# Optimization experiments

Measured on AMD Instinct MI355X. Metric: run time of the kernel, lower is better.

The kernel has to match this reference:

```python
import jax, jax.numpy as jnp
import numpy as np

B, T, IN_DIM, H, W = 32, 20, 3, 1, 256
HID = 64
FC1_IN = HID * T * H * W  # 327680
FC1_OUT = 512
OUT_DIM = 3


def setup_inputs() -> dict:
    key = jax.random.key(0)
    ks = jax.random.split(key, 6)
    s = 0.02
    return dict(
        x=jax.random.normal(ks[0], (B, T, IN_DIM, H, W), dtype=jnp.float32),
        conv_w0=jax.random.normal(ks[1], (4 * HID, IN_DIM + HID, 3, 3), dtype=jnp.float32) * s,
        conv_b0=jnp.zeros((4 * HID,), dtype=jnp.float32),
        conv_w1=jax.random.normal(ks[2], (4 * HID, HID + HID, 3, 3), dtype=jnp.float32) * s,
        conv_b1=jnp.zeros((4 * HID,), dtype=jnp.float32),
        fc1_w=jax.random.normal(ks[3], (FC1_OUT, FC1_IN), dtype=jnp.float32) * s,
        fc1_b=jnp.zeros((FC1_OUT,), dtype=jnp.float32),
        fc2_w=jax.random.normal(ks[4], (OUT_DIM, FC1_OUT), dtype=jnp.float32) * s,
        fc2_b=jnp.zeros((OUT_DIM,), dtype=jnp.float32),
    )


def _convlstm_layer(inp, w, b):
    # inp: (B, T, C, H, W); w: (4*hid, C+hid, kh, kw)
    Bn, Tn, C, Hn, Wn = inp.shape
    hid = w.shape[0] // 4
    h0 = jnp.zeros((Bn, hid, Hn, Wn), inp.dtype)

    def step(carry, x_t):
        h, c = carry
        z = jnp.concatenate([x_t, h], axis=1)  # (B, C+hid, H, W)
        gates = jax.lax.conv_general_dilated(
            z, w, window_strides=(1, 1), padding='SAME',
            dimension_numbers=('NCHW', 'OIHW', 'NCHW')) + b[None, :, None, None]
        i, f, o, g = jnp.split(gates, 4, axis=1)
        c_new = jax.nn.sigmoid(f) * c + jax.nn.sigmoid(i) * jnp.tanh(g)
        h_new = jax.nn.sigmoid(o) * jnp.tanh(c_new)
        return (h_new, c_new), h_new

    _, hs = jax.lax.scan(step, (h0, h0), jnp.swapaxes(inp, 0, 1))
    return jnp.swapaxes(hs, 0, 1)  # (B, T, hid, H, W)


def reference(x, conv_w0, conv_b0, conv_w1, conv_b1, fc1_w, fc1_b, fc2_w, fc2_b):
    h = _convlstm_layer(x, conv_w0, conv_b0)
    h = _convlstm_layer(h, conv_w1, conv_b1)
    flat = h.reshape(h.shape[0], -1)  # (B, T*hid*H*W), torch .view order
    z = jax.nn.relu(flat @ fc1_w.T + fc1_b)
    out = z @ fc2_w.T + fc2_b
    return jnp.concatenate([out[:, :2], jax.nn.sigmoid(out[:, 2:])], axis=1)
```

## Files before the change

kernel.cpp:

```cpp
#include <hip/hip_runtime.h>
#include <hip/hip_bf16.h>
#include <cstddef>

#define BATCH 32
#define TSTEPS 20
#define IN_DIM 3
#define WIDTH 256
#define HID 64
#define FC1_IN 327680
#define FC1_OUT 512
#define OUT_DIM 3

#define MARG 8
#define REGC 48
#define CORE 8
#define ROWS 50
#define CROWS 48

#define KSLICE 1280
#define KPHASE 640
#define NSPLIT 256

typedef _Float16 half8 __attribute__((ext_vector_type(8)));
typedef float floatx4 __attribute__((ext_vector_type(4)));

__device__ __forceinline__ float sigm(float x) {
    return 1.0f / (1.0f + __expf(-x));
}
__device__ __forceinline__ float tanh_fast(float x) {
    return 1.0f - 2.0f / (__expf(2.0f * x) + 1.0f);
}


__global__ __launch_bounds__(256) void prep_w0(
    const float* __restrict__ cw0, _Float16* __restrict__ wt0)
{
    int e = blockIdx.x * 256 + threadIdx.x;
    if (e >= 256 * 96) return;
    int co = e / 96, cip = e - co * 96;
    int ci = (cip < 64) ? (3 + cip) : (cip < 67 ? cip - 64 : -1);
    float v[3] = {0.f, 0.f, 0.f};
    if (ci >= 0) {
#pragma unroll
        for (int kw = 0; kw < 3; ++kw)
            v[kw] = cw0[(size_t)(co * 67 + ci) * 9 + 3 + kw];
    }
#pragma unroll
    for (int kw = 0; kw < 3; ++kw)
        wt0[(size_t)(kw * 256 + co) * 96 + cip] = (_Float16)v[kw];
}

__global__ __launch_bounds__(256) void prep_w1(
    const float* __restrict__ cw1, _Float16* __restrict__ wt1)
{
    int e = blockIdx.x * 256 + threadIdx.x;
    int co = e >> 7, ci = e & 127;
#pragma unroll
    for (int kw = 0; kw < 3; ++kw)
        wt1[(size_t)(kw * 256 + co) * 128 + ci] =
            (_Float16)cw1[(size_t)(co * 128 + ci) * 9 + 3 + kw];
}

__global__ __launch_bounds__(256) void prep_x(
    const float* __restrict__ x, _Float16* __restrict__ xT)
{
    int e = blockIdx.x * 256 + threadIdx.x;
    if (e >= TSTEPS * BATCH * WIDTH) return;
    int t = e / (BATCH * WIDTH);
    int rem = e - t * BATCH * WIDTH;
    int b = rem >> 8, w = rem & 255;
    half8 v = {};
#pragma unroll
    for (int ci = 0; ci < 3; ++ci)
        v[ci] = (_Float16)x[(size_t)((b * TSTEPS + t) * IN_DIM + ci) * WIDTH + w];
    *(half8*)&xT[(size_t)e * 8] = v;
}

__global__ __launch_bounds__(512) void conv_chunk(
    const _Float16* __restrict__ xT,
    const _Float16* __restrict__ wt0,
    const _Float16* __restrict__ wt1,
    const float* __restrict__ cb0,
    const float* __restrict__ cb1,
    _Float16* __restrict__ fcin,
    _Float16* __restrict__ h0g,
    _Float16* __restrict__ h1g,
    float* __restrict__ c0g,
    float* __restrict__ c1g,
    int t0, int first, int save, int nst)
{
    __shared__ __align__(16) _Float16 h0s[2][ROWS * 64];
    __shared__ __align__(16) _Float16 h1s[2][ROWS * 64];
    __shared__ __align__(16) _Float16 xs[2][ROWS * 8];
    __shared__ float c0s[CROWS * 64];
    __shared__ float c1s[CROWS * 64];
    __shared__ __align__(16) _Float16 zero16[8];

    const int b    = blockIdx.x;
    const int w0   = blockIdx.y * 32;
    const int tid  = threadIdx.x;
    const int wave = tid >> 6;
    const int ln = tid & 63;
    const int lr = ln & 15;
    const int kg = ln >> 4;

    {
        _Float16* h0f = &h0s[0][0];
        _Float16* h1f = &h1s[0][0];
        for (int i = tid; i < 2 * ROWS * 64; i += 512) { h0f[i] = (_Float16)0.0f; h1f[i] = (_Float16)0.0f; }
        for (int i = tid; i < CROWS * 64; i += 512) { c0s[i] = 0.0f; c1s[i] = 0.0f; }
        for (int i = tid; i < ROWS * 8; i += 512) xs[1][i] = (_Float16)0.0f;
        if (tid < 8) zero16[tid] = (_Float16)0.0f;
    }
    __syncthreads();

    {
        if (tid < ROWS) {
            int w = w0 - 9 + tid;
            half8 v = {};
            if (w >= 0 && w < WIDTH)
                v = *(const half8*)&xT[((size_t)(t0 * BATCH + b) * WIDTH + w) * 8];
            *(half8*)&xs[0][tid * 8] = v;
        }
        if (!first) {
            for (int i = tid; i < REGC * 8; i += 512) {
                int row = 1 + (i >> 3), c = i & 7;
                int w = w0 - 9 + row;
                half8 v0 = {}, v1 = {};
                if (w >= 0 && w < WIDTH) {
                    v0 = *(const half8*)&h0g[((size_t)b * WIDTH + w) * 64 + c * 8];
                    v1 = *(const half8*)&h1g[((size_t)b * WIDTH + w) * 64 + c * 8];
                }
                int phys = c ^ (row & 7);
                *(half8*)&h0s[1][row * 64 + phys * 8] = v0;
                *(half8*)&h1s[1][row * 64 + phys * 8] = v1;
            }
            for (int i = tid; i < REGC * 64; i += 512) {
                int n = i >> 6, hc = i & 63;
                int w = w0 - 8 + n;
                float v0 = 0.f, v1 = 0.f;
                if (w >= 0 && w < WIDTH) {
                    v0 = c0g[((size_t)b * WIDTH + w) * 64 + hc];
                    v1 = c1g[((size_t)b * WIDTH + w) * 64 + hc];
                }
                int ci = n * 64 + (hc ^ (((n >> 2) & 3) << 4));
                c0s[ci] = v0;
                c1s[ci] = v1;
            }
        }
    }

    if (wave < 4) {
        const int hc = wave * 16 + lr;

        half8 b0r[3][3][4];
#pragma unroll
        for (int kw = 0; kw < 3; ++kw)
#pragma unroll
        for (int kf = 0; kf < 3; ++kf)
#pragma unroll
        for (int cf = 0; cf < 4; ++cf)
            b0r[kw][kf][cf] = *(const half8*)&wt0[
                (size_t)(kw * 256 + cf * 64 + hc) * 96 + kf * 32 + kg * 8];

        float cbr0[4];
#pragma unroll
        for (int cf = 0; cf < 4; ++cf) cbr0[cf] = cb0[cf * 64 + hc];

        __syncthreads();

        for (int p = 0; p <= nst; ++p) {
            const int rd = (p ^ 1) & 1;
            const int wr = p & 1;
            half8 xreg = {};
            const bool xst = (p < nst - 1) && (tid < ROWS);
            if (xst) {
                int w = w0 - 9 + tid;
                if (w >= 0 && w < WIDTH)
                    xreg = *(const half8*)&xT[((size_t)((t0 + p + 1) * BATCH + b) * WIDTH + w) * 8];
            }
            if (p < nst) {
#pragma unroll
                for (int j = 0; j < 3; ++j) {
                    floatx4 acc[4];
#pragma unroll
                    for (int cf = 0; cf < 4; ++cf) acc[cf] = (floatx4)0.0f;
                    __builtin_amdgcn_s_setprio(1);
#pragma unroll
                    for (int kw = 0; kw < 3; ++kw)
#pragma unroll
                    for (int kf = 0; kf < 3; ++kf) {
                        int row = 16 * j + lr + kw;
                        half8 a;
                        if (kf < 2) {
                            int phys = (kf * 4 + kg) ^ (row & 7);
                            a = *(const half8*)&h0s[rd][row * 64 + phys * 8];
                        } else {
                            a = (kg == 0) ? *(const half8*)&xs[wr][row * 8]
                                          : *(const half8*)&zero16[0];
                        }
#pragma unroll
                        for (int cf = 0; cf < 4; ++cf)
                            acc[cf] = __builtin_amdgcn_mfma_f32_16x16x32_f16(a, b0r[kw][kf][cf], acc[cf], 0, 0, 0);
                    }
                    __builtin_amdgcn_s_setprio(0);
#pragma unroll
                    for (int r = 0; r < 4; ++r) {
                        int n = 16 * j + kg * 4 + r;
                        int cidx = n * 64 + (hc ^ (kg << 4));
                        float cv = c0s[cidx];
                        float cn = sigm(acc[1][r] + cbr0[1]) * cv
                                 + sigm(acc[0][r] + cbr0[0]) * tanh_fast(acc[3][r] + cbr0[3]);
                        c0s[cidx] = cn;
                        int w = w0 - 8 + n;
                        if (w >= 0 && w < WIDTH) {
                            _Float16 hv = (_Float16)(sigm(acc[2][r] + cbr0[2]) * tanh_fast(cn));
                            int rowo = n + 1;
                            int phys = (hc >> 3) ^ (rowo & 7);
                            *((_Float16*)((char*)&h0s[wr][0] + rowo * 128 + phys * 16 + (hc & 7) * 2)) = hv;
                        }
                    }
                }
            }
            if (xst) *(half8*)&xs[(p + 1) & 1][tid * 8] = xreg;
            __syncthreads();
        }
    } else {
        const int hc = (wave - 4) * 16 + lr;

        half8 b1r[3][4][4];
#pragma unroll
        for (int kw = 0; kw < 3; ++kw)
#pragma unroll
        for (int kf = 0; kf < 4; ++kf)
#pragma unroll
        for (int cf = 0; cf < 4; ++cf)
            b1r[kw][kf][cf] = *(const half8*)&wt1[
                (size_t)(kw * 256 + cf * 64 + hc) * 128 + kf * 32 + kg * 8];

        float cbr1[4];
#pragma unroll
        for (int cf = 0; cf < 4; ++cf) cbr1[cf] = cb1[cf * 64 + hc];

        __syncthreads();

        for (int p = 0; p <= nst; ++p) {
            const int rd   = (p ^ 1) & 1;
            const int h1rd = p & 1;
            if (p >= 1) {
#pragma unroll
                for (int j = 0; j < 3; ++j) {
                    floatx4 acc[4];
#pragma unroll
                    for (int cf = 0; cf < 4; ++cf) acc[cf] = (floatx4)0.0f;
                    __builtin_amdgcn_s_setprio(1);
#pragma unroll
                    for (int kw = 0; kw < 3; ++kw)
#pragma unroll
                    for (int kf = 0; kf < 4; ++kf) {
                        int row = 16 * j + lr + kw;
                        half8 a;
                        if (kf < 2) {
                            int phys = (kf * 4 + kg) ^ (row & 7);
                            a = *(const half8*)&h0s[rd][row * 64 + phys * 8];
                        } else {
                            int phys = ((kf - 2) * 4 + kg) ^ (row & 7);
                            a = *(const half8*)&h1s[h1rd][row * 64 + phys * 8];
                        }
#pragma unroll
                        for (int cf = 0; cf < 4; ++cf)
                            acc[cf] = __builtin_amdgcn_mfma_f32_16x16x32_f16(a, b1r[kw][kf][cf], acc[cf], 0, 0, 0);
                    }
                    __builtin_amdgcn_s_setprio(0);
#pragma unroll
                    for (int r = 0; r < 4; ++r) {
                        int n = 16 * j + kg * 4 + r;
                        int cidx = n * 64 + (hc ^ (kg << 4));
                        float cv = c1s[cidx];
                        float cn = sigm(acc[1][r] + cbr1[1]) * cv
                                 + sigm(acc[0][r] + cbr1[0]) * tanh_fast(acc[3][r] + cbr1[3]);
                        c1s[cidx] = cn;
                        _Float16 hv = (_Float16)(sigm(acc[2][r] + cbr1[2]) * tanh_fast(cn));
                        int w = w0 - 8 + n;
                        if (w >= 0 && w < WIDTH) {
                            int rowo = n + 1;
                            int phys = (hc >> 3) ^ (rowo & 7);
                            *((_Float16*)((char*)&h1s[rd][0] + rowo * 128 + phys * 16 + (hc & 7) * 2)) = hv;
                        }
                        if (n >= CORE && n < CORE + 32)
                            fcin[(size_t)b * FC1_IN + (size_t)((t0 + p - 1) * HID + hc) * WIDTH + w] = hv;
                    }
                }
            }
            __syncthreads();
        }
    }

    if (save) {
        for (int i = tid; i < 32 * 64; i += 512) {
            int n = CORE + (i >> 6);
            int hc = i & 63;
            int w = w0 + (i >> 6);
            int rowo = n + 1;
            int physh = (hc >> 3) ^ (rowo & 7);
            h0g[((size_t)b * WIDTH + w) * 64 + hc] = h0s[0][rowo * 64 + physh * 8 + (hc & 7)];
            h1g[((size_t)b * WIDTH + w) * 64 + hc] = h1s[0][rowo * 64 + physh * 8 + (hc & 7)];
            int ci = n * 64 + (hc ^ (((n >> 2) & 3) << 4));
            c0g[((size_t)b * WIDTH + w) * 64 + hc] = c0s[ci];
            c1g[((size_t)b * WIDTH + w) * 64 + hc] = c1s[ci];
        }
    }
}

__global__ __launch_bounds__(1024) void fc1_mfma(
    const _Float16* __restrict__ a,
    const float* __restrict__ w,
    float* __restrict__ part)
{
    __shared__ _Float16 alds[32 * 648];

    const int blk = blockIdx.x;
    const int tid = threadIdx.x;
    const int wv  = tid >> 6;
    const int ln  = tid & 63;
    const int lg  = ln >> 4;
    const int lr  = ln & 15;
    const int k0  = blk * KSLICE;

    floatx4 acc[2][2];
#pragma unroll
    for (int bt = 0; bt < 2; ++bt)
#pragma unroll
        for (int nt = 0; nt < 2; ++nt) acc[bt][nt] = (floatx4)0.0f;

    const float* wbase[2];
#pragma unroll
    for (int nt = 0; nt < 2; ++nt)
        wbase[nt] = w + (size_t)(wv * 32 + nt * 16 + lr) * FC1_IN + k0 + lg * 8;

    for (int p = 0; p < 2; ++p) {
        __syncthreads();
        for (int i = tid; i < 32 * 80; i += 1024) {
            int r = i / 80;
            int c = (i - r * 80) * 8;
            *(half8*)&alds[r * 648 + c] =
                *(const half8*)&a[(size_t)r * FC1_IN + k0 + p * KPHASE + c];
        }
        __syncthreads();

        for (int kc = 0; kc < KPHASE / 32; ++kc) {
            half8 af0 = *(const half8*)&alds[lr * 648 + kc * 32 + lg * 8];
            half8 af1 = *(const half8*)&alds[(16 + lr) * 648 + kc * 32 + lg * 8];
#pragma unroll
            for (int nt = 0; nt < 2; ++nt) {
                const float* wp = wbase[nt] + p * KPHASE + kc * 32;
                float4 wlo = *(const float4*)wp;
                float4 whi = *(const float4*)(wp + 4);
                half8 bf;
                bf[0] = (_Float16)wlo.x; bf[1] = (_Float16)wlo.y;
                bf[2] = (_Float16)wlo.z; bf[3] = (_Float16)wlo.w;
                bf[4] = (_Float16)whi.x; bf[5] = (_Float16)whi.y;
                bf[6] = (_Float16)whi.z; bf[7] = (_Float16)whi.w;
                acc[0][nt] = __builtin_amdgcn_mfma_f32_16x16x32_f16(af0, bf, acc[0][nt], 0, 0, 0);
                acc[1][nt] = __builtin_amdgcn_mfma_f32_16x16x32_f16(af1, bf, acc[1][nt], 0, 0, 0);
            }
        }
    }

#pragma unroll
    for (int bt = 0; bt < 2; ++bt)
#pragma unroll
        for (int nt = 0; nt < 2; ++nt) {
            int n = wv * 32 + nt * 16 + lr;
            int b = bt * 16 + lg * 4;
            *(float4*)&part[((size_t)blk * FC1_OUT + n) * BATCH + b] =
                *(float4*)&acc[bt][nt];
        }
}

__global__ __launch_bounds__(256) void fc1_reduce(
    const float* __restrict__ part, const float* __restrict__ b1,
    float* __restrict__ z1)
{
    int e = blockIdx.x * 256 + threadIdx.x;
    float s = 0.0f;
    for (int ks = 0; ks < NSPLIT; ++ks)
        s += part[(size_t)ks * (FC1_OUT * BATCH) + e];
    int n = e >> 5, b = e & 31;
    float v = s + b1[n];
    z1[(size_t)b * FC1_OUT + n] = v > 0.0f ? v : 0.0f;
}

__global__ __launch_bounds__(128) void fc2_kernel(
    const float* __restrict__ z1, const float* __restrict__ w2,
    const float* __restrict__ b2, float* __restrict__ out)
{
    int t = threadIdx.x;
    if (t >= BATCH * OUT_DIM) return;
    int b = t / OUT_DIM, n = t - b * OUT_DIM;
    const float* zr = z1 + (size_t)b * FC1_OUT;
    const float* wr = w2 + (size_t)n * FC1_OUT;
    float acc = b2[n];
    for (int k = 0; k < FC1_OUT; ++k) acc += zr[k] * wr[k];
    if (n == 2) acc = sigm(acc);
    out[(size_t)b * OUT_DIM + n] = acc;
}

extern "C" void kernel_launch(void* const* d_in, const int* in_sizes, int n_in,
                              void* d_out, int out_size, void* d_ws, size_t ws_size,
                              hipStream_t stream) {
    const float* x   = (const float*)d_in[0];
    const float* cw0 = (const float*)d_in[1];
    const float* cb0 = (const float*)d_in[2];
    const float* cw1 = (const float*)d_in[3];
    const float* cb1 = (const float*)d_in[4];
    const float* w1  = (const float*)d_in[5];
    const float* b1  = (const float*)d_in[6];
    const float* w2  = (const float*)d_in[7];
    const float* b2  = (const float*)d_in[8];
    float* out = (float*)d_out;

    const size_t S = (size_t)BATCH * WIDTH * HID;
    char* p = (char*)d_ws;
    auto alloc = [&](size_t bytes) { char* r = p; p += (bytes + 255) & ~(size_t)255; return r; };

    _Float16* wt0  = (_Float16*)alloc((size_t)3 * 256 * 96 * 2);
    _Float16* wt1  = (_Float16*)alloc((size_t)3 * 256 * 128 * 2);
    _Float16* xT   = (_Float16*)alloc((size_t)TSTEPS * BATCH * WIDTH * 8 * 2);
    _Float16* fcin = (_Float16*)alloc((size_t)BATCH * FC1_IN * 2);
    _Float16* h0g  = (_Float16*)alloc(S * 2);
    _Float16* h1g  = (_Float16*)alloc(S * 2);
    float*    c0g  = (float*)alloc(S * 4);
    float*    c1g  = (float*)alloc(S * 4);
    float*    part = (float*)alloc((size_t)NSPLIT * FC1_OUT * BATCH * 4);
    float*    z1   = (float*)alloc((size_t)BATCH * FC1_OUT * 4);

    prep_w0<<<96, 256, 0, stream>>>(cw0, wt0);
    prep_w1<<<128, 256, 0, stream>>>(cw1, wt1);
    prep_x<<<(TSTEPS * BATCH * WIDTH + 255) / 256, 256, 0, stream>>>(x, xT);

    const int t0s[3]  = {0, 7, 14};
    const int nsts[3] = {7, 7, 6};
    for (int k = 0; k < 3; ++k) {
        conv_chunk<<<dim3(BATCH, 8), 512, 0, stream>>>(
            xT, wt0, wt1, cb0, cb1, fcin, h0g, h1g, c0g, c1g,
            t0s[k], (k == 0) ? 1 : 0, (k < 2) ? 1 : 0, nsts[k]);
    }

    fc1_mfma<<<NSPLIT, 1024, 0, stream>>>(fcin, w1, part);
    fc1_reduce<<<64, 256, 0, stream>>>(part, b1, z1);
    fc2_kernel<<<1, 128, 0, stream>>>(z1, w2, b2, out);
}
```

Before: 398.6 us.

## Stage fc1 weights through swizzled LDS with register prefetch, 512 threads per block

The fc1 kernel now loads the weight slice with fully coalesced float4 row reads into registers, converts them to fp16 and writes them into an XOR-swizzled LDS tile. The next 64-column chunk is prefetched while the current one is consumed. The whole activation slice is loaded into LDS once instead of in two phases. Blocks shrink to 512 threads, each wave covering 64 output rows, and the per-block LDS footprint grows a lot, which may limit occupancy.

```diff
diff --git a/kernel.cpp b/kernel.cpp
--- a/kernel.cpp
+++ b/kernel.cpp
@@ -18,10 +18,11 @@
 #define CROWS 48
 
 #define KSLICE 1280
-#define KPHASE 640
 #define NSPLIT 256
+#define ALDS_STR 1288
 
 typedef _Float16 half8 __attribute__((ext_vector_type(8)));
+typedef _Float16 half4 __attribute__((ext_vector_type(4)));
 typedef float floatx4 __attribute__((ext_vector_type(4)));
 
 __device__ __forceinline__ float sigm(float x) {
@@ -312,12 +313,13 @@
     }
 }
 
-__global__ __launch_bounds__(1024) void fc1_mfma(
+__global__ __launch_bounds__(512) void fc1_mfma(
     const _Float16* __restrict__ a,
     const float* __restrict__ w,
     float* __restrict__ part)
 {
-    __shared__ _Float16 alds[32 * 648];
+    __shared__ _Float16 alds[32 * ALDS_STR];
+    __shared__ __align__(16) _Float16 blds[512 * 64];
 
     const int blk = blockIdx.x;
     const int tid = threadIdx.x;
@@ -327,40 +329,61 @@
     const int lr  = ln & 15;
     const int k0  = blk * KSLICE;
 
-    floatx4 acc[2][2];
+    for (int i = tid; i < 32 * 160; i += 512) {
+        int r = i / 160;
+        int c = (i - r * 160) * 8;
+        *(half8*)&alds[r * ALDS_STR + c] =
+            *(const half8*)&a[(size_t)r * FC1_IN + k0 + c];
+    }
+
+    const float4* w4 = (const float4*)w;
+    const int lrow = ln >> 4;
+    const int lcol = ln & 15;
+
+    float4 rr[16];
+#pragma unroll
+    for (int i = 0; i < 16; ++i) {
+        int row = wv * 64 + i * 4 + lrow;
+        rr[i] = w4[(size_t)row * (FC1_IN / 4) + (size_t)(k0 >> 2) + lcol];
+    }
+
+    floatx4 acc[2][4];
 #pragma unroll
     for (int bt = 0; bt < 2; ++bt)
 #pragma unroll
-        for (int nt = 0; nt < 2; ++nt) acc[bt][nt] = (floatx4)0.0f;
-
-    const float* wbase[2];
-#pragma unroll
-    for (int nt = 0; nt < 2; ++nt)
-        wbase[nt] = w + (size_t)(wv * 32 + nt * 16 + lr) * FC1_IN + k0 + lg * 8;
-
-    for (int p = 0; p < 2; ++p) {
+        for (int nt = 0; nt < 4; ++nt) acc[bt][nt] = (floatx4)0.0f;
+
+    for (int cc = 0; cc < 20; ++cc) {
         __syncthreads();
-        for (int i = tid; i < 32 * 80; i += 1024) {
-            int r = i / 80;
-            int c = (i - r * 80) * 8;
-            *(half8*)&alds[r * 648 + c] =
-                *(const half8*)&a[(size_t)r * FC1_IN + k0 + p * KPHASE + c];
+#pragma unroll
+        for (int i = 0; i < 16; ++i) {
+            int row = wv * 64 + i * 4 + lrow;
+            int c = lcol >> 1, h = lcol & 1;
+            int phys = c ^ (row & 7);
+            half4 hv;
+            hv[0] = (_Float16)rr[i].x; hv[1] = (_Float16)rr[i].y;
+            hv[2] = (_Float16)rr[i].z; hv[3] = (_Float16)rr[i].w;
+            *(half4*)((char*)blds + row * 128 + phys * 16 + h * 8) = hv;
+        }
+        if (cc < 19) {
+#pragma unroll
+            for (int i = 0; i < 16; ++i) {
+                int row = wv * 64 + i * 4 + lrow;
+                rr[i] = w4[(size_t)row * (FC1_IN / 4)
+                           + (size_t)((k0 + (cc + 1) * 64) >> 2) + lcol];
+            }
         }
         __syncthreads();
-
-        for (int kc = 0; kc < KPHASE / 32; ++kc) {
-            half8 af0 = *(const half8*)&alds[lr * 648 + kc * 32 + lg * 8];
-            half8 af1 = *(const half8*)&alds[(16 + lr) * 648 + kc * 32 + lg * 8];
-#pragma unroll
-            for (int nt = 0; nt < 2; ++nt) {
-                const float* wp = wbase[nt] + p * KPHASE + kc * 32;
-                float4 wlo = *(const float4*)wp;
-                float4 whi = *(const float4*)(wp + 4);
-                half8 bf;
-                bf[0] = (_Float16)wlo.x; bf[1] = (_Float16)wlo.y;
-                bf[2] = (_Float16)wlo.z; bf[3] = (_Float16)wlo.w;
-                bf[4] = (_Float16)whi.x; bf[5] = (_Float16)whi.y;
-                bf[6] = (_Float16)whi.z; bf[7] = (_Float16)whi.w;
+#pragma unroll
+        for (int kc2 = 0; kc2 < 2; ++kc2) {
+            int kk = cc * 64 + kc2 * 32 + lg * 8;
+            half8 af0 = *(const half8*)&alds[lr * ALDS_STR + kk];
+            half8 af1 = *(const half8*)&alds[(16 + lr) * ALDS_STR + kk];
+#pragma unroll
+            for (int nt = 0; nt < 4; ++nt) {
+                int row = wv * 64 + nt * 16 + lr;
+                int phys = (kc2 * 4 + lg) ^ (row & 7);
+                half8 bf = *(const half8*)((const char*)blds + row * 128 + phys * 16);
                 acc[0][nt] = __builtin_amdgcn_mfma_f32_16x16x32_f16(af0, bf, acc[0][nt], 0, 0, 0);
                 acc[1][nt] = __builtin_amdgcn_mfma_f32_16x16x32_f16(af1, bf, acc[1][nt], 0, 0, 0);
             }
@@ -370,8 +393,8 @@
 #pragma unroll
     for (int bt = 0; bt < 2; ++bt)
 #pragma unroll
-        for (int nt = 0; nt < 2; ++nt) {
-            int n = wv * 32 + nt * 16 + lr;
+        for (int nt = 0; nt < 4; ++nt) {
+            int n = wv * 64 + nt * 16 + lr;
             int b = bt * 16 + lg * 4;
             *(float4*)&part[((size_t)blk * FC1_OUT + n) * BATCH + b] =
                 *(float4*)&acc[bt][nt];
@@ -447,7 +470,7 @@
             t0s[k], (k == 0) ? 1 : 0, (k < 2) ? 1 : 0, nsts[k]);
     }
 
-    fc1_mfma<<<NSPLIT, 1024, 0, stream>>>(fcin, w1, part);
+    fc1_mfma<<<NSPLIT, 512, 0, stream>>>(fcin, w1, part);
     fc1_reduce<<<64, 256, 0, stream>>>(part, b1, z1);
     fc2_kernel<<<1, 128, 0, stream>>>(z1, w2, b2, out);
 }
```

Measured after the change: 394.7 us. About the same (-1.0%).
